# Kernel tuning notes

Hardware: AMD Instinct MI355X
Metric: run time of the kernel (lower is better)

The kernel has to match this reference:

```python
import jax, jax.numpy as jnp
import numpy as np

B, NV, FD = 16, 128, 8192
T_TEMP = 0.2      # self.T
MARGIN = 1.0      # nn.TripletMarginLoss default
EPS = 1e-6        # pairwise_distance eps


def _l2norm(x):
    # torch F.normalize(dim=1): x / max(||x||, 1e-12)
    nrm = jnp.maximum(jnp.linalg.norm(x, axis=-1, keepdims=True), 1e-12)
    return x / nrm


def _ssl_parts(qb, kb, nb, num_gt):
    # qb,kb,nb: [NV, FD] flattened reid embeddings for one image
    qv = _l2norm(qb)[:num_gt]          # [g, FD]
    kv = _l2norm(kb)[:num_gt]          # [g, FD]
    nv = _l2norm(nb)                   # [NV, FD] (negatives are NOT sliced)
    g = num_gt
    S = qv @ kv.T                      # [g, g] all pairwise dots (replaces torch.dot loops)
    # similarity-matrix loss
    sm = jnp.sum((S - jnp.eye(g, dtype=S.dtype)) ** 2) / (g * g)
    # pairwise distances with torch eps convention: ||a - b + eps||_2
    # = sqrt(||a||^2 + ||b||^2 - 2 a.b + 2*eps*(sum(a)-sum(b)) + D*eps^2); ||a||=||b||=1
    sq = qv.sum(axis=1)                # [g]
    sk = kv.sum(axis=1)                # [g]
    const = FD * EPS * EPS
    d_qk = jnp.sqrt(jnp.maximum(2.0 - 2.0 * S + 2.0 * EPS * (sq[:, None] - sk[None, :]) + const, 0.0))
    d_kq = jnp.sqrt(jnp.maximum(2.0 - 2.0 * S.T + 2.0 * EPS * (sk[:, None] - sq[None, :]) + const, 0.0))
    off = 1.0 - jnp.eye(g, dtype=S.dtype)
    # triplet: anc=q_i,pos=k_i,neg=k_j  and  anc=k_i,pos=q_i,neg=q_j, j != i
    tri1 = jnp.sum(jax.nn.relu(jnp.diag(d_qk)[:, None] - d_qk + MARGIN) * off)
    tri2 = jnp.sum(jax.nn.relu(jnp.diag(d_kq)[:, None] - d_kq + MARGIN) * off)
    tri_sum = tri1 + tri2
    # cycle consistency: |q_i.k_j - k_i.q_j| = |S[i,j] - S[j,i]|
    cyc = jnp.sum(jnp.abs(S - S.T) * off) / (g * (g - 1))
    # InfoNCE: l_pos = q_i.k_i, l_neg = q @ n.T
    l_pos = jnp.diag(S)[:, None]       # [g, 1]
    l_neg = qv @ nv.T                  # [g, NV]
    logits = jnp.concatenate([l_pos, l_neg], axis=1) / T_TEMP
    ce = jnp.mean(jax.nn.logsumexp(logits, axis=1) - logits[:, 0])  # CE with labels=0
    return sm, tri_sum, cyc, ce / g


def setup_inputs() -> dict:
    key = jax.random.key(0)
    kq, kk, kn = jax.random.split(key, 3)
    q = jax.random.normal(kq, (B, NV, FD), dtype=jnp.float32)
    k = jax.random.normal(kk, (B, NV, FD), dtype=jnp.float32)
    n = jax.random.normal(kn, (B, NV, FD), dtype=jnp.float32)
    return {"q": q, "k": k, "n": n, "num_gt": NV}


def reference(q, k, n, num_gt):
    sm, tri, cyc, ce = jax.vmap(lambda a, b, c: _ssl_parts(a, b, c, num_gt))(q, k, n)
    tri_cnt = 2 * num_gt * (num_gt - 1)
    # original bug: tri_loss accumulates across batches while tri_cnt resets,
    # so each batch contributes cumsum(tri)[b] / tri_cnt
    ssl = jnp.sum(sm) + jnp.sum(jnp.cumsum(tri)) / tri_cnt + jnp.sum(cyc) + jnp.sum(ce)
    return ssl
```

## Files before the change

kernel.cpp:

```cpp
#include <hip/hip_runtime.h>
#include <cstdint>
#include <cstddef>

#define B_N   16
#define G_N   128
#define FD_N  8192
#define KSPLIT 16
#define KC    512
#define BK    64
#define NSTAGE 8

typedef unsigned short u16;
typedef u16  u16x8 __attribute__((ext_vector_type(8)));
typedef __bf16 bf16x8 __attribute__((ext_vector_type(8)));
typedef float f32x16 __attribute__((ext_vector_type(16)));

#define QSUM_P   0
#define QSSQ_P   32768
#define KSUM_P   65536
#define KSSQ_P   98304
#define NSSQ_P   131072
#define SM_ROW   163840
#define CE_ROW   165888
#define S_OFF    167936
#define PART_OFF_F 430080

__device__ __forceinline__ u16 f2bf(float f) {
    uint32_t u = __float_as_uint(f);
    u += 0x7FFFu + ((u >> 16) & 1u);
    return (u16)(u >> 16);
}

#define LGKM0_BAR() do { asm volatile("s_waitcnt lgkmcnt(0)" ::: "memory"); \
                         __builtin_amdgcn_s_barrier(); } while (0)

__global__ __launch_bounds__(512, 2)
void k_gemm(const float* __restrict__ q, const float* __restrict__ kM,
            const float* __restrict__ nM, float* __restrict__ ws)
{
    __shared__ __align__(16) u16 smem[2 * 24576];

    const int tid = threadIdx.x;
    const int blk = blockIdx.x;
    const int b   = blk >> 4;
    const int kch = blk & 15;

    const int lane  = tid & 63;
    const int wv    = tid >> 6;
    const int wm    = wv >> 2;
    const int wn    = wv & 3;
    const int khalf = lane >> 5;
    const int lrow  = lane & 31;
    const int g     = lane >> 4;
    const int cc    = lane & 15;

    const size_t mat_off = (size_t)b * (G_N * FD_N) + (size_t)kch * KC;
    const float* Ap = q + mat_off;
    const float* Bw = (wv < 4 ? kM : nM) + mat_off;

    float4 La[4], Lb[8];
    float sA_[4] = {0,0,0,0}, qA_[4] = {0,0,0,0};
    float sB_[8] = {0,0,0,0,0,0,0,0}, qB_[8] = {0,0,0,0,0,0,0,0};

    f32x16 acc[2][2];
    #pragma unroll
    for (int m = 0; m < 2; ++m)
      #pragma unroll
      for (int n = 0; n < 2; ++n)
        #pragma unroll
        for (int e = 0; e < 16; ++e) acc[m][n][e] = 0.f;

#define ISSUE(S) do {                                                          \
        const size_t ko_ = (size_t)((S)*BK + cc*4);                            \
        _Pragma("unroll")                                                      \
        for (int i = 0; i < 4; ++i)                                            \
            La[i] = *(const float4*)(Ap + (size_t)(wv*16 + i*4 + g)*FD_N + ko_); \
        _Pragma("unroll")                                                      \
        for (int i = 0; i < 8; ++i)                                            \
            Lb[i] = *(const float4*)(Bw + (size_t)(wn*32 + i*4 + g)*FD_N + ko_); \
    } while (0)

#define CVTWRITE(BUF) do {                                                     \
        u16* dA_ = smem + (BUF)*24576;                                         \
        u16* dB_ = dA_ + 8192;                                                 \
        _Pragma("unroll")                                                      \
        for (int i = 0; i < 4; ++i) {                                          \
            const int r_ = wv*16 + i*4 + g;                                    \
            float4 v = La[i];                                                  \
            sA_[i] += (v.x + v.y) + (v.z + v.w);                               \
            qA_[i] += v.x*v.x + v.y*v.y + v.z*v.z + v.w*v.w;                   \
            uint2 p;                                                           \
            p.x = (uint32_t)f2bf(v.x) | ((uint32_t)f2bf(v.y) << 16);           \
            p.y = (uint32_t)f2bf(v.z) | ((uint32_t)f2bf(v.w) << 16);           \
            *(uint2*)(dA_ + r_*64 + ((cc ^ ((r_&7)<<1)) << 2)) = p;            \
        }                                                                      \
        _Pragma("unroll")                                                      \
        for (int i = 0; i < 8; ++i) {                                          \
            const int r_  = wn*32 + i*4 + g;                                   \
            const int rl_ = r_ + (wv < 4 ? 0 : 128);                           \
            float4 v = Lb[i];                                                  \
            sB_[i] += (v.x + v.y) + (v.z + v.w);                               \
            qB_[i] += v.x*v.x + v.y*v.y + v.z*v.z + v.w*v.w;                   \
            uint2 p;                                                           \
            p.x = (uint32_t)f2bf(v.x) | ((uint32_t)f2bf(v.y) << 16);           \
            p.y = (uint32_t)f2bf(v.z) | ((uint32_t)f2bf(v.w) << 16);           \
            *(uint2*)(dB_ + rl_*64 + ((cc ^ ((rl_&7)<<1)) << 2)) = p;          \
        }                                                                      \
    } while (0)

#define FRAG(DP, R, KCH)                                                       \
    __builtin_bit_cast(bf16x8, *(const u16x8*)((DP) + (R)*64 +                 \
        ((((KCH)*2 + khalf) ^ ((R)&7)) << 3)))

#define COMPUTE(BUF) do {                                                      \
        const u16* dA_ = smem + (BUF)*24576;                                   \
        const u16* dB_ = dA_ + 8192;                                           \
        __builtin_amdgcn_s_setprio(1);                                         \
        _Pragma("unroll")                                                      \
        for (int kc = 0; kc < 4; ++kc) {                                       \
            bf16x8 a0_ = FRAG(dA_, wm*64 +      lrow, kc);                     \
            bf16x8 a1_ = FRAG(dA_, wm*64 + 32 + lrow, kc);                     \
            bf16x8 b0_ = FRAG(dB_, wn*64 +      lrow, kc);                     \
            bf16x8 b1_ = FRAG(dB_, wn*64 + 32 + lrow, kc);                     \
            acc[0][0] = __builtin_amdgcn_mfma_f32_32x32x16_bf16(a0_, b0_, acc[0][0], 0,0,0); \
            acc[0][1] = __builtin_amdgcn_mfma_f32_32x32x16_bf16(a0_, b1_, acc[0][1], 0,0,0); \
            acc[1][0] = __builtin_amdgcn_mfma_f32_32x32x16_bf16(a1_, b0_, acc[1][0], 0,0,0); \
            acc[1][1] = __builtin_amdgcn_mfma_f32_32x32x16_bf16(a1_, b1_, acc[1][1], 0,0,0); \
        }                                                                      \
        __builtin_amdgcn_s_setprio(0);                                         \
    } while (0)

    ISSUE(0);
    CVTWRITE(0);
    LGKM0_BAR();

    for (int s = 0; s < NSTAGE; ++s) {
        if (s + 1 < NSTAGE) ISSUE(s + 1);
        COMPUTE(s & 1);
        if (s + 1 < NSTAGE) {
            LGKM0_BAR();
            CVTWRITE((s + 1) & 1);
            LGKM0_BAR();
        }
    }

    u16* part = (u16*)(ws + PART_OFF_F);
    #pragma unroll
    for (int m = 0; m < 2; ++m)
      #pragma unroll
      for (int n = 0; n < 2; ++n) {
        const int colg = wn*64 + n*32 + lrow;
        const int ho   = colg >> 7;
        const int col  = colg & 127;
        u16* pb = part + (size_t)(b*2 + ho) * 262144;
        const int rbase = wm*64 + m*32 + 4*khalf;
        #pragma unroll
        for (int reg = 0; reg < 16; ++reg) {
            const int row = rbase + (reg & 3) + 8*(reg >> 2);
            pb[(row*16 + kch)*128 + col] = f2bf(acc[m][n][reg]);
        }
      }

    #pragma unroll
    for (int i = 0; i < 4; ++i)
        #pragma unroll
        for (int msk = 8; msk >= 1; msk >>= 1) {
            sA_[i] += __shfl_xor(sA_[i], msk, 64);
            qA_[i] += __shfl_xor(qA_[i], msk, 64);
        }
    #pragma unroll
    for (int i = 0; i < 8; ++i)
        #pragma unroll
        for (int msk = 8; msk >= 1; msk >>= 1) {
            sB_[i] += __shfl_xor(sB_[i], msk, 64);
            qB_[i] += __shfl_xor(qB_[i], msk, 64);
        }
    if (cc == 0) {
        #pragma unroll
        for (int i = 0; i < 4; ++i) {
            const int o = kch*2048 + b*G_N + (wv*16 + i*4 + g);
            ws[QSUM_P + o] = sA_[i]; ws[QSSQ_P + o] = qA_[i];
        }
        #pragma unroll
        for (int i = 0; i < 8; ++i) {
            const int o = kch*2048 + b*G_N + (wn*32 + i*4 + g);
            if (wv < 4) { ws[KSUM_P + o] = sB_[i]; ws[KSSQ_P + o] = qB_[i]; }
            else        { ws[NSSQ_P + o] = qB_[i]; }
        }
    }
#undef ISSUE
#undef CVTWRITE
#undef FRAG
#undef COMPUTE
}

__global__ __launch_bounds__(256)
void k_red2(float* __restrict__ ws, float* __restrict__ out)
{
    const int blk  = blockIdx.x;
    const int b    = blk >> 4;
    const int half = (blk >> 3) & 1;
    const int rg   = blk & 7;
    const int t    = threadIdx.x;
    const int lr   = t >> 4;
    const int i    = rg*16 + lr;
    const int c8   = t & 15;
    __shared__ float nrm[128];
    __shared__ float invq_s[16];

    if (blk == 0 && t == 0) out[0] = 0.f;

    if (t < 128) {
        float ss = 0.f;
        const float* p = ws + (half ? NSSQ_P : KSSQ_P) + b*G_N + t;
        #pragma unroll
        for (int kc2 = 0; kc2 < KSPLIT; ++kc2) ss += p[kc2*2048];
        nrm[t] = 1.f / fmaxf(sqrtf(ss), 1e-12f);
    } else if (t < 144) {
        float ss = 0.f;
        const float* p = ws + QSSQ_P + b*G_N + rg*16 + (t - 128);
        #pragma unroll
        for (int kc2 = 0; kc2 < KSPLIT; ++kc2) ss += p[kc2*2048];
        invq_s[t-128] = 1.f / fmaxf(sqrtf(ss), 1e-12f);
    }
    __syncthreads();

    const u16* part = (const u16*)(ws + PART_OFF_F) + (size_t)(b*2 + half) * 262144;
    float s[8] = {0,0,0,0,0,0,0,0};
    #pragma unroll
    for (int kc2 = 0; kc2 < KSPLIT; ++kc2) {
        u16x8 h = *(const u16x8*)(part + (size_t)(i*16 + kc2)*128 + c8*8);
        #pragma unroll
        for (int e = 0; e < 8; ++e)
            s[e] += __uint_as_float(((uint32_t)h[e]) << 16);
    }
    const float iq = invq_s[lr];
    if (half == 0) {
        float smacc = 0.f;
        float S8[8];
        #pragma unroll
        for (int e = 0; e < 8; ++e) {
            int j = c8*8 + e;
            S8[e] = s[e] * iq * nrm[j];
            float d = S8[e] - (j == i ? 1.f : 0.f);
            smacc += d*d;
        }
        float* Sp = ws + S_OFF + (size_t)b*16384 + i*G_N + c8*8;
        float4 w0 = {S8[0],S8[1],S8[2],S8[3]};
        float4 w1 = {S8[4],S8[5],S8[6],S8[7]};
        *(float4*)Sp = w0; *(float4*)(Sp+4) = w1;
        #pragma unroll
        for (int m = 8; m >= 1; m >>= 1) smacc += __shfl_xor(smacc, m, 64);
        if (c8 == 0) ws[SM_ROW + b*G_N + i] = smacc;
    } else {
        float eacc = 0.f;
        #pragma unroll
        for (int e = 0; e < 8; ++e)
            eacc += __expf(5.f * s[e] * iq * nrm[c8*8+e]);
        #pragma unroll
        for (int m = 8; m >= 1; m >>= 1) eacc += __shfl_xor(eacc, m, 64);
        if (c8 == 0) ws[CE_ROW + b*G_N + i] = eacc;
    }
}

__global__ __launch_bounds__(256)
void k_epi(float* __restrict__ ws, float* __restrict__ out)
{
    const int blk = blockIdx.x;
    const int b   = blk >> 3;
    const int i0  = (blk & 7) * 16;
    const int t   = threadIdx.x;
    __shared__ float sqv[128], skv[128], ddq[128], ddk[128];
    __shared__ float rbuf[4];
    const float c0 = (float)FD_N * 1e-6f * 1e-6f;

    const float* S = ws + S_OFF + (size_t)b * 16384;
    if (t < 128) {
        float qs=0, qq=0, ks=0, kq=0;
        #pragma unroll
        for (int kc2 = 0; kc2 < KSPLIT; ++kc2) {
            int o = kc2*2048 + b*G_N + t;
            qs += ws[QSUM_P + o]; qq += ws[QSSQ_P + o];
            ks += ws[KSUM_P + o]; kq += ws[KSSQ_P + o];
        }
        float iq = 1.f/fmaxf(sqrtf(qq),1e-12f);
        float ik = 1.f/fmaxf(sqrtf(kq),1e-12f);
        float sq = qs*iq, sk = ks*ik;
        sqv[t]=sq; skv[t]=sk;
        float Stt = S[t*G_N + t];
        ddq[t] = sqrtf(fmaxf(2.f - 2.f*Stt + 2e-6f*(sq-sk) + c0, 0.f));
        ddk[t] = sqrtf(fmaxf(2.f - 2.f*Stt + 2e-6f*(sk-sq) + c0, 0.f));
    }
    __syncthreads();

    float tri=0.f, cyc=0.f, ce=0.f, sm=0.f;
    #pragma unroll
    for (int p = 0; p < 8; ++p) {
        int idx = p*256 + t;
        int i = i0 + (idx >> 7), j = idx & 127;
        if (i != j) {
            float S_ij = S[i*G_N + j];
            float dqk = sqrtf(fmaxf(2.f - 2.f*S_ij + 2e-6f*(sqv[i]-skv[j]) + c0, 0.f));
            tri += fmaxf(ddq[i] - dqk + 1.f, 0.f);
            float dkq = sqrtf(fmaxf(2.f - 2.f*S_ij + 2e-6f*(skv[j]-sqv[i]) + c0, 0.f));
            tri += fmaxf(ddk[j] - dkq + 1.f, 0.f);
            cyc += fabsf(S_ij - S[j*G_N + i]);
        }
    }
    if (t < 16) {
        int r = i0 + t;
        float lp = 5.f * S[r*G_N + r];
        ce = __logf(ws[CE_ROW + b*G_N + r] + __expf(lp)) - lp;
        sm = ws[SM_ROW + b*G_N + r];
    }
    float contrib = sm * (1.f/16384.f) + cyc * (1.f/16256.f) + ce * (1.f/16384.f)
                  + (float)(B_N - b) * tri * (1.f/32512.f);
    #pragma unroll
    for (int m = 32; m >= 1; m >>= 1) contrib += __shfl_xor(contrib, m, 64);
    if ((t & 63) == 0) rbuf[t >> 6] = contrib;
    __syncthreads();
    if (t == 0) atomicAdd(out, rbuf[0] + rbuf[1] + rbuf[2] + rbuf[3]);
}

extern "C" void kernel_launch(void* const* d_in, const int* in_sizes, int n_in,
                              void* d_out, int out_size, void* d_ws, size_t ws_size,
                              hipStream_t stream)
{
    const float* q  = (const float*)d_in[0];
    const float* kM = (const float*)d_in[1];
    const float* nM = (const float*)d_in[2];
    float* ws  = (float*)d_ws;
    float* out = (float*)d_out;

    k_gemm<<<B_N * KSPLIT, 512, 0, stream>>>(q, kM, nM, ws);
    k_red2<<<256, 256, 0, stream>>>(ws, out);
    k_epi<<<128, 256, 0, stream>>>(ws, out);
}
```

Before: 220.0 us.

## Fuse split-K reduction and epilogue into one per-batch kernel with LDS S

Merges the split-K partial reduction kernel and the epilogue kernel into a single kernel that runs one 1024-thread block per batch. The similarity matrix stays in LDS instead of a global workspace round trip, and one kernel launch is dropped. The output zeroing moves into the GEMM kernel. In exchange, only 16 blocks run the reduction, so parallelism is much lower than the previous 256+128 blocks.

```diff
diff --git a/kernel.cpp b/kernel.cpp
--- a/kernel.cpp
+++ b/kernel.cpp
@@ -20,9 +20,6 @@
 #define KSUM_P   65536
 #define KSSQ_P   98304
 #define NSSQ_P   131072
-#define SM_ROW   163840
-#define CE_ROW   165888
-#define S_OFF    167936
 #define PART_OFF_F 430080
 
 __device__ __forceinline__ u16 f2bf(float f) {
@@ -36,7 +33,8 @@
 
 __global__ __launch_bounds__(512, 2)
 void k_gemm(const float* __restrict__ q, const float* __restrict__ kM,
-            const float* __restrict__ nM, float* __restrict__ ws)
+            const float* __restrict__ nM, float* __restrict__ ws,
+            float* __restrict__ out)
 {
     __shared__ __align__(16) u16 smem[2 * 24576];
 
@@ -44,6 +42,8 @@
     const int blk = blockIdx.x;
     const int b   = blk >> 4;
     const int kch = blk & 15;
+
+    if (blk == 0 && tid == 0) out[0] = 0.f;
 
     const int lane  = tid & 63;
     const int wv    = tid >> 6;
@@ -194,132 +194,132 @@
 #undef COMPUTE
 }
 
-__global__ __launch_bounds__(256)
-void k_red2(float* __restrict__ ws, float* __restrict__ out)
+__global__ __launch_bounds__(1024)
+void k_fin(float* __restrict__ ws, float* __restrict__ out)
 {
-    const int blk  = blockIdx.x;
-    const int b    = blk >> 4;
-    const int half = (blk >> 3) & 1;
-    const int rg   = blk & 7;
-    const int t    = threadIdx.x;
-    const int lr   = t >> 4;
-    const int i    = rg*16 + lr;
-    const int c8   = t & 15;
-    __shared__ float nrm[128];
-    __shared__ float invq_s[16];
-
-    if (blk == 0 && t == 0) out[0] = 0.f;
+    __shared__ float S_lds[G_N * G_N];
+    __shared__ float invq[128], nrk[128], nrn[128], sqv[128], skv[128];
+    __shared__ float ddq[128], ddk[128], smrow[128], cerow[128];
+    __shared__ float wred[16];
+
+    const int b = blockIdx.x;
+    const int t = threadIdx.x;
+    const float c0 = (float)FD_N * 1e-6f * 1e-6f;
 
     if (t < 128) {
-        float ss = 0.f;
-        const float* p = ws + (half ? NSSQ_P : KSSQ_P) + b*G_N + t;
-        #pragma unroll
-        for (int kc2 = 0; kc2 < KSPLIT; ++kc2) ss += p[kc2*2048];
-        nrm[t] = 1.f / fmaxf(sqrtf(ss), 1e-12f);
-    } else if (t < 144) {
-        float ss = 0.f;
-        const float* p = ws + QSSQ_P + b*G_N + rg*16 + (t - 128);
-        #pragma unroll
-        for (int kc2 = 0; kc2 < KSPLIT; ++kc2) ss += p[kc2*2048];
-        invq_s[t-128] = 1.f / fmaxf(sqrtf(ss), 1e-12f);
-    }
-    __syncthreads();
-
-    const u16* part = (const u16*)(ws + PART_OFF_F) + (size_t)(b*2 + half) * 262144;
-    float s[8] = {0,0,0,0,0,0,0,0};
-    #pragma unroll
-    for (int kc2 = 0; kc2 < KSPLIT; ++kc2) {
-        u16x8 h = *(const u16x8*)(part + (size_t)(i*16 + kc2)*128 + c8*8);
-        #pragma unroll
-        for (int e = 0; e < 8; ++e)
-            s[e] += __uint_as_float(((uint32_t)h[e]) << 16);
-    }
-    const float iq = invq_s[lr];
-    if (half == 0) {
-        float smacc = 0.f;
-        float S8[8];
-        #pragma unroll
-        for (int e = 0; e < 8; ++e) {
-            int j = c8*8 + e;
-            S8[e] = s[e] * iq * nrm[j];
-            float d = S8[e] - (j == i ? 1.f : 0.f);
-            smacc += d*d;
-        }
-        float* Sp = ws + S_OFF + (size_t)b*16384 + i*G_N + c8*8;
-        float4 w0 = {S8[0],S8[1],S8[2],S8[3]};
-        float4 w1 = {S8[4],S8[5],S8[6],S8[7]};
-        *(float4*)Sp = w0; *(float4*)(Sp+4) = w1;
-        #pragma unroll
-        for (int m = 8; m >= 1; m >>= 1) smacc += __shfl_xor(smacc, m, 64);
-        if (c8 == 0) ws[SM_ROW + b*G_N + i] = smacc;
-    } else {
-        float eacc = 0.f;
-        #pragma unroll
-        for (int e = 0; e < 8; ++e)
-            eacc += __expf(5.f * s[e] * iq * nrm[c8*8+e]);
-        #pragma unroll
-        for (int m = 8; m >= 1; m >>= 1) eacc += __shfl_xor(eacc, m, 64);
-        if (c8 == 0) ws[CE_ROW + b*G_N + i] = eacc;
-    }
-}
-
-__global__ __launch_bounds__(256)
-void k_epi(float* __restrict__ ws, float* __restrict__ out)
-{
-    const int blk = blockIdx.x;
-    const int b   = blk >> 3;
-    const int i0  = (blk & 7) * 16;
-    const int t   = threadIdx.x;
-    __shared__ float sqv[128], skv[128], ddq[128], ddk[128];
-    __shared__ float rbuf[4];
-    const float c0 = (float)FD_N * 1e-6f * 1e-6f;
-
-    const float* S = ws + S_OFF + (size_t)b * 16384;
-    if (t < 128) {
-        float qs=0, qq=0, ks=0, kq=0;
-        #pragma unroll
-        for (int kc2 = 0; kc2 < KSPLIT; ++kc2) {
-            int o = kc2*2048 + b*G_N + t;
+        float qs=0.f, qq=0.f, ks=0.f, kq=0.f, nq=0.f;
+        #pragma unroll
+        for (int kc = 0; kc < KSPLIT; ++kc) {
+            const int o = kc*2048 + b*G_N + t;
             qs += ws[QSUM_P + o]; qq += ws[QSSQ_P + o];
             ks += ws[KSUM_P + o]; kq += ws[KSSQ_P + o];
-        }
-        float iq = 1.f/fmaxf(sqrtf(qq),1e-12f);
-        float ik = 1.f/fmaxf(sqrtf(kq),1e-12f);
-        float sq = qs*iq, sk = ks*ik;
-        sqv[t]=sq; skv[t]=sk;
-        float Stt = S[t*G_N + t];
-        ddq[t] = sqrtf(fmaxf(2.f - 2.f*Stt + 2e-6f*(sq-sk) + c0, 0.f));
-        ddk[t] = sqrtf(fmaxf(2.f - 2.f*Stt + 2e-6f*(sk-sq) + c0, 0.f));
+            nq += ws[NSSQ_P + o];
+        }
+        const float iq = 1.f / fmaxf(sqrtf(qq), 1e-12f);
+        const float ik = 1.f / fmaxf(sqrtf(kq), 1e-12f);
+        invq[t] = iq; nrk[t] = ik;
+        nrn[t]  = 1.f / fmaxf(sqrtf(nq), 1e-12f);
+        sqv[t]  = qs * iq; skv[t] = ks * ik;
     }
     __syncthreads();
 
-    float tri=0.f, cyc=0.f, ce=0.f, sm=0.f;
-    #pragma unroll
-    for (int p = 0; p < 8; ++p) {
-        int idx = p*256 + t;
-        int i = i0 + (idx >> 7), j = idx & 127;
-        if (i != j) {
-            float S_ij = S[i*G_N + j];
-            float dqk = sqrtf(fmaxf(2.f - 2.f*S_ij + 2e-6f*(sqv[i]-skv[j]) + c0, 0.f));
-            tri += fmaxf(ddq[i] - dqk + 1.f, 0.f);
-            float dkq = sqrtf(fmaxf(2.f - 2.f*S_ij + 2e-6f*(skv[j]-sqv[i]) + c0, 0.f));
-            tri += fmaxf(ddk[j] - dkq + 1.f, 0.f);
-            cyc += fabsf(S_ij - S[j*G_N + i]);
-        }
-    }
-    if (t < 16) {
-        int r = i0 + t;
-        float lp = 5.f * S[r*G_N + r];
-        ce = __logf(ws[CE_ROW + b*G_N + r] + __expf(lp)) - lp;
-        sm = ws[SM_ROW + b*G_N + r];
-    }
-    float contrib = sm * (1.f/16384.f) + cyc * (1.f/16256.f) + ce * (1.f/16384.f)
+    const int i  = t >> 3;
+    const int c8 = t & 7;
+    const int j0 = c8 * 16;
+    const u16* part = (const u16*)(ws + PART_OFF_F);
+    const float iqv = invq[i];
+
+    {
+        float s[16];
+        #pragma unroll
+        for (int e = 0; e < 16; ++e) s[e] = 0.f;
+        const u16* p0 = part + (size_t)(b*2) * 262144 + i*2048 + j0;
+        #pragma unroll
+        for (int kc = 0; kc < KSPLIT; ++kc) {
+            const u16x8 h0 = *(const u16x8*)(p0 + kc*128);
+            const u16x8 h1 = *(const u16x8*)(p0 + kc*128 + 8);
+            #pragma unroll
+            for (int e = 0; e < 8; ++e) {
+                s[e]   += __uint_as_float(((uint32_t)h0[e]) << 16);
+                s[e+8] += __uint_as_float(((uint32_t)h1[e]) << 16);
+            }
+        }
+        float sm = 0.f;
+        #pragma unroll
+        for (int e = 0; e < 16; ++e) {
+            const int j = j0 + e;
+            const float Sv = s[e] * iqv * nrk[j];
+            S_lds[i*G_N + j] = Sv;
+            const float d = Sv - (j == i ? 1.f : 0.f);
+            sm += d*d;
+        }
+        #pragma unroll
+        for (int m = 4; m >= 1; m >>= 1) sm += __shfl_xor(sm, m, 64);
+        if (c8 == 0) smrow[i] = sm;
+    }
+    {
+        float s[16];
+        #pragma unroll
+        for (int e = 0; e < 16; ++e) s[e] = 0.f;
+        const u16* p1 = part + (size_t)(b*2 + 1) * 262144 + i*2048 + j0;
+        #pragma unroll
+        for (int kc = 0; kc < KSPLIT; ++kc) {
+            const u16x8 h0 = *(const u16x8*)(p1 + kc*128);
+            const u16x8 h1 = *(const u16x8*)(p1 + kc*128 + 8);
+            #pragma unroll
+            for (int e = 0; e < 8; ++e) {
+                s[e]   += __uint_as_float(((uint32_t)h0[e]) << 16);
+                s[e+8] += __uint_as_float(((uint32_t)h1[e]) << 16);
+            }
+        }
+        float ea = 0.f;
+        #pragma unroll
+        for (int e = 0; e < 16; ++e)
+            ea += __expf(5.f * s[e] * iqv * nrn[j0 + e]);
+        #pragma unroll
+        for (int m = 4; m >= 1; m >>= 1) ea += __shfl_xor(ea, m, 64);
+        if (c8 == 0) cerow[i] = ea;
+    }
+    __syncthreads();
+
+    if (t < 128) {
+        const float Stt = S_lds[t*G_N + t];
+        ddq[t] = sqrtf(fmaxf(2.f - 2.f*Stt + 2e-6f*(sqv[t] - skv[t]) + c0, 0.f));
+        ddk[t] = sqrtf(fmaxf(2.f - 2.f*Stt + 2e-6f*(skv[t] - sqv[t]) + c0, 0.f));
+    }
+    __syncthreads();
+
+    float tri = 0.f, cyc = 0.f, rowterm = 0.f;
+    #pragma unroll
+    for (int p2 = 0; p2 < 16; ++p2) {
+        const int idx = p2*1024 + t;
+        const int ii = idx >> 7, jj = idx & 127;
+        if (ii != jj) {
+            const float S_ij = S_lds[ii*G_N + jj];
+            const float dqk = sqrtf(fmaxf(2.f - 2.f*S_ij + 2e-6f*(sqv[ii]-skv[jj]) + c0, 0.f));
+            tri += fmaxf(ddq[ii] - dqk + 1.f, 0.f);
+            const float dkq = sqrtf(fmaxf(2.f - 2.f*S_ij + 2e-6f*(skv[jj]-sqv[ii]) + c0, 0.f));
+            tri += fmaxf(ddk[jj] - dkq + 1.f, 0.f);
+            cyc += fabsf(S_ij - S_lds[jj*G_N + ii]);
+        }
+    }
+    if (t < 128) {
+        const float lp = 5.f * S_lds[t*G_N + t];
+        const float ce = __logf(cerow[t] + __expf(lp)) - lp;
+        rowterm = smrow[t] * (1.f/16384.f) + ce * (1.f/16384.f);
+    }
+    float contrib = rowterm + cyc * (1.f/16256.f)
                   + (float)(B_N - b) * tri * (1.f/32512.f);
     #pragma unroll
     for (int m = 32; m >= 1; m >>= 1) contrib += __shfl_xor(contrib, m, 64);
-    if ((t & 63) == 0) rbuf[t >> 6] = contrib;
+    if ((t & 63) == 0) wred[t >> 6] = contrib;
     __syncthreads();
-    if (t == 0) atomicAdd(out, rbuf[0] + rbuf[1] + rbuf[2] + rbuf[3]);
+    if (t == 0) {
+        float tot = 0.f;
+        #pragma unroll
+        for (int w = 0; w < 16; ++w) tot += wred[w];
+        atomicAdd(out, tot);
+    }
 }
 
 extern "C" void kernel_launch(void* const* d_in, const int* in_sizes, int n_in,
@@ -332,7 +332,6 @@
     float* ws  = (float*)d_ws;
     float* out = (float*)d_out;
 
-    k_gemm<<<B_N * KSPLIT, 512, 0, stream>>>(q, kM, nM, ws);
-    k_red2<<<256, 256, 0, stream>>>(ws, out);
-    k_epi<<<128, 256, 0, stream>>>(ws, out);
+    k_gemm<<<B_N * KSPLIT, 512, 0, stream>>>(q, kM, nM, ws, out);
+    k_fin<<<B_N, 1024, 0, stream>>>(ws, out);
 }
```

Result: slower. 230.5 us (+4.8%).
